# Kernel optimization log

Hardware: AMD Instinct MI355X
Metric: run time of the kernel (lower is better)

## Reference

```python
import jax, jax.numpy as jnp
from jax import lax
import numpy as np

B, L, D = 32, 128, 6          # programs, statements per program, tree depth
T = 2 ** D - 1                # nodes per statement tree (complete binary tree)
V, E, C, H = 50000, 128, 128, 256  # vocab, embed dim, encode dim, gru hidden


def setup_inputs():
    key = jax.random.key(0)
    ks = jax.random.split(key, 12)
    s = 0.05
    return {
        "tokens": jax.random.randint(ks[0], (B, L, T), 0, V),
        "emb": jax.random.normal(ks[1], (V, E), jnp.float32) * s,
        "Wc": jax.random.normal(ks[2], (C, E), jnp.float32) * s,
        "bc": jax.random.normal(ks[3], (C,), jnp.float32) * s,
        "Wih_f": jax.random.normal(ks[4], (3 * H, C), jnp.float32) * s,
        "Whh_f": jax.random.normal(ks[5], (3 * H, H), jnp.float32) * s,
        "bih_f": jax.random.normal(ks[6], (3 * H,), jnp.float32) * s,
        "bhh_f": jax.random.normal(ks[7], (3 * H,), jnp.float32) * s,
        "Wih_b": jax.random.normal(ks[8], (3 * H, C), jnp.float32) * s,
        "Whh_b": jax.random.normal(ks[9], (3 * H, H), jnp.float32) * s,
        "bih_b": jax.random.normal(ks[10], (3 * H,), jnp.float32) * s,
        "bhh_b": jax.random.normal(ks[11], (3 * H,), jnp.float32) * s,
    }


def _tree_encode(tokens, emb, Wc, bc):
    # h(node) = W_c(embed(tok)) + sum of children subtree encodings (W_l/W_r unused in source)
    h = jnp.einsum("blte,ce->bltc", emb[tokens], Wc) + bc  # [B,L,T,C]
    for d in range(D - 1, 0, -1):  # deepest level first
        start, n = 2 ** d - 1, 2 ** d
        ch = h[:, :, start:start + n, :]
        ch = ch.reshape(ch.shape[0], ch.shape[1], n // 2, 2, ch.shape[-1]).sum(3)
        p0 = 2 ** (d - 1) - 1
        h = h.at[:, :, p0:p0 + n // 2, :].add(ch)
    # max over all subtree encodings, with zeros included (batch_node starts at 0)
    return jnp.maximum(h.max(axis=2), 0.0)  # [B,L,C]


def _gru_dir(x, Wih, Whh, bih, bhh, reverse):
    # torch GRU gate order: r, z, n
    def step(hp, xt):
        gi = xt @ Wih.T + bih
        gh = hp @ Whh.T + bhh
        ir, iz, inn = jnp.split(gi, 3, -1)
        hr, hz, hn = jnp.split(gh, 3, -1)
        r = jax.nn.sigmoid(ir + hr)
        z = jax.nn.sigmoid(iz + hz)
        nn_ = jnp.tanh(inn + r * hn)
        hnew = (1.0 - z) * nn_ + z * hp
        return hnew, hnew
    xs = jnp.swapaxes(x, 0, 1)  # [L,B,C]
    h0 = jnp.zeros((x.shape[0], Whh.shape[1]), x.dtype)
    _, ys = lax.scan(step, h0, xs, reverse=reverse)
    return jnp.swapaxes(ys, 0, 1)  # [B,L,H]


def reference(tokens, emb, Wc, bc, Wih_f, Whh_f, bih_f, bhh_f, Wih_b, Whh_b, bih_b, bhh_b):
    enc = _tree_encode(tokens, emb, Wc, bc)                       # [B,L,C]
    fwd = _gru_dir(enc, Wih_f, Whh_f, bih_f, bhh_f, reverse=False)
    bwd = _gru_dir(enc, Wih_b, Whh_b, bih_b, bhh_b, reverse=True)
    gru_out = jnp.concatenate([fwd, bwd], axis=-1)                # [B,L,2H]
    return gru_out.max(axis=1)                                    # max-pool over time -> [B,2H]
```

## Files before the change

kernel.cpp:

```cpp
#include <hip/hip_runtime.h>
#include <hip/hip_bf16.h>
#include <hip/hip_fp16.h>
#include <math.h>

#define NV 50000
#define NE 128
#define NC 128
#define NH 256
#define NB 32
#define NL 128
#define NT 63
#define G3 768

typedef _Float16 half2_t __attribute__((ext_vector_type(2)));

__device__ __forceinline__ float sigmoidf_(float x) { return 1.0f / (1.0f + expf(-x)); }

__device__ __forceinline__ float fdot2_(unsigned int a, unsigned int b, float c) {
#if __has_builtin(__builtin_amdgcn_fdot2)
  return __builtin_amdgcn_fdot2(__builtin_bit_cast(half2_t, a),
                                __builtin_bit_cast(half2_t, b), c, false);
#else
  half2_t ah = __builtin_bit_cast(half2_t, a);
  half2_t bh = __builtin_bit_cast(half2_t, b);
  return fmaf((float)ah[0], (float)bh[0], fmaf((float)ah[1], (float)bh[1], c));
#endif
}

__global__ __launch_bounds__(256) void gemm_bt_k128(
    const float* __restrict__ A, const float* __restrict__ Bm,
    const float* __restrict__ bias, float* __restrict__ Cm,
    int M, int N) {
  __shared__ __align__(16) float As[64 * 129];
  __shared__ __align__(16) float BsT[128 * 132];
  const int m0 = blockIdx.x * 64;
  const int n0 = blockIdx.y * 128;
  const int tid = threadIdx.x;

#pragma unroll
  for (int i = 0; i < 32; ++i) {
    int e = tid + i * 256;
    int r = e >> 7, k = e & 127;
    int m = m0 + r;
    As[r * 129 + k] = (m < M) ? A[(size_t)m * 128 + k] : 0.0f;
  }
#pragma unroll
  for (int i = 0; i < 64; ++i) {
    int e = tid + i * 256;
    int n = e >> 7, k = e & 127;
    BsT[k * 132 + n] = Bm[(size_t)(n0 + n) * 128 + k];
  }
  __syncthreads();

  const int tn = tid & 15;
  const int tm = tid >> 4;
  const int ml = tm * 4, nl = tn * 8;

  float acc[4][8];
#pragma unroll
  for (int i = 0; i < 4; ++i)
#pragma unroll
    for (int j = 0; j < 8; ++j) acc[i][j] = 0.0f;

#pragma unroll 4
  for (int k = 0; k < 128; ++k) {
    float a0 = As[(ml + 0) * 129 + k];
    float a1 = As[(ml + 1) * 129 + k];
    float a2 = As[(ml + 2) * 129 + k];
    float a3 = As[(ml + 3) * 129 + k];
    float4 b0 = *(const float4*)&BsT[k * 132 + nl];
    float4 b1 = *(const float4*)&BsT[k * 132 + nl + 4];
    const float bv[8] = {b0.x, b0.y, b0.z, b0.w, b1.x, b1.y, b1.z, b1.w};
#pragma unroll
    for (int j = 0; j < 8; ++j) {
      acc[0][j] = fmaf(a0, bv[j], acc[0][j]);
      acc[1][j] = fmaf(a1, bv[j], acc[1][j]);
      acc[2][j] = fmaf(a2, bv[j], acc[2][j]);
      acc[3][j] = fmaf(a3, bv[j], acc[3][j]);
    }
  }

  float bv[8];
#pragma unroll
  for (int j = 0; j < 8; ++j) bv[j] = bias ? bias[n0 + nl + j] : 0.0f;

#pragma unroll
  for (int i = 0; i < 4; ++i) {
    int m = m0 + ml + i;
    if (m < M) {
      float* crow = &Cm[(size_t)m * N + n0 + nl];
#pragma unroll
      for (int j = 0; j < 8; ++j) crow[j] = acc[i][j] + bv[j];
    }
  }
}

__global__ __launch_bounds__(128) void tree_encode(
    const int* __restrict__ tokens, const float* __restrict__ P,
    const float* __restrict__ bc, float* __restrict__ enc) {
  __shared__ int toks[NT];
  const int blk = blockIdx.x;
  const int c = threadIdx.x;
  if (c < NT) toks[c] = tokens[(size_t)blk * NT + c];
  __syncthreads();

  float s[NT];
#pragma unroll
  for (int i = 0; i < NT; ++i) s[i] = P[(size_t)toks[i] * NC + c];
#pragma unroll
  for (int i = 30; i >= 0; --i) s[i] += s[2 * i + 1] + s[2 * i + 2];

  const float bcv = bc[c];
  float m = -1e30f;
#pragma unroll
  for (int i = 0; i < NT; ++i) {
    const float cnt = (i == 0) ? 63.0f
                    : (i < 3)  ? 31.0f
                    : (i < 7)  ? 15.0f
                    : (i < 15) ? 7.0f
                    : (i < 31) ? 3.0f
                               : 1.0f;
    m = fmaxf(m, s[i] + cnt * bcv);
  }
  enc[(size_t)blk * NC + c] = fmaxf(m, 0.0f);
}

__global__ __launch_bounds__(256) void conv_w_f16(
    const float* __restrict__ Wf, const float* __restrict__ Wb,
    unsigned int* __restrict__ out) {
  int i = blockIdx.x * 256 + threadIdx.x;
  if (i < G3 * (NH / 2)) {
    float2 a = ((const float2*)Wf)[i];
    __half2 ha = __floats2half2_rn(a.x, a.y);
    out[i] = *(unsigned int*)&ha;
    float2 b = ((const float2*)Wb)[i];
    __half2 hb = __floats2half2_rn(b.x, b.y);
    out[G3 * (NH / 2) + i] = *(unsigned int*)&hb;
  }
}

__global__ __launch_bounds__(768, 3) void gru_scan_reg(
    const unsigned int* __restrict__ Wh16, const float* __restrict__ GI,
    const float* __restrict__ bhh_f, const float* __restrict__ bhh_b,
    float* __restrict__ out) {
  const int dir = blockIdx.x >> 5;
  const int b = blockIdx.x & 31;
  const int tid = threadIdx.x;

  __shared__ __align__(16) unsigned int h16p[NH / 2];
  __shared__ float gh[G3];

  unsigned int w[128];
  {
    const uint4* wrow = (const uint4*)(Wh16 + ((size_t)dir * G3 + tid) * (NH / 2));
#pragma unroll
    for (int i = 0; i < 32; ++i) {
      uint4 v = wrow[i];
      w[4 * i + 0] = v.x; w[4 * i + 1] = v.y;
      w[4 * i + 2] = v.z; w[4 * i + 3] = v.w;
    }
  }

  const float* __restrict__ bhh = dir ? bhh_b : bhh_f;
  float br = 0.f, bz = 0.f, bn = 0.f, hreg = 0.f, hmax = -1e30f;
  if (tid < NH) {
    br = bhh[tid];
    bz = bhh[tid + NH];
    bn = bhh[tid + 2 * NH];
  }
  if (tid < NH / 2) h16p[tid] = 0u;
  const float* __restrict__ gi_base =
      GI + ((size_t)dir * NB * NL + (size_t)b * NL) * G3;
  __syncthreads();

  for (int st = 0; st < NL; ++st) {
    const int t = dir ? (NL - 1 - st) : st;
    float gir = 0.f, giz = 0.f, gin = 0.f;
    if (tid < NH) {
      const float* gi = gi_base + (size_t)t * G3;
      gir = gi[tid];
      giz = gi[tid + NH];
      gin = gi[tid + 2 * NH];
    }
    float acc = 0.0f;
    const uint4* h4 = (const uint4*)h16p;
#pragma unroll
    for (int k = 0; k < 32; ++k) {
      uint4 hv = h4[k];
      acc = fdot2_(w[4 * k + 0], hv.x, acc);
      acc = fdot2_(w[4 * k + 1], hv.y, acc);
      acc = fdot2_(w[4 * k + 2], hv.z, acc);
      acc = fdot2_(w[4 * k + 3], hv.w, acc);
    }
    gh[tid] = acc;
    __syncthreads();
    if (tid < NH) {
      float r = sigmoidf_(gir + gh[tid] + br);
      float z = sigmoidf_(giz + gh[tid + NH] + bz);
      float n = tanhf(gin + r * (gh[tid + 2 * NH] + bn));
      hreg = (1.0f - z) * n + z * hreg;
      hmax = fmaxf(hmax, hreg);
      ((unsigned short*)h16p)[tid] = __half_as_ushort(__float2half_rn(hreg));
    }
    __syncthreads();
  }
  if (tid < NH) out[(size_t)b * (2 * NH) + (size_t)dir * NH + tid] = hmax;
}

extern "C" void kernel_launch(void* const* d_in, const int* in_sizes, int n_in,
                              void* d_out, int out_size, void* d_ws, size_t ws_size,
                              hipStream_t stream) {
  const int*   tokens = (const int*)d_in[0];
  const float* emb    = (const float*)d_in[1];
  const float* Wc     = (const float*)d_in[2];
  const float* bc     = (const float*)d_in[3];
  const float* Wih_f  = (const float*)d_in[4];
  const float* Whh_f  = (const float*)d_in[5];
  const float* bih_f  = (const float*)d_in[6];
  const float* bhh_f  = (const float*)d_in[7];
  const float* Wih_b  = (const float*)d_in[8];
  const float* Whh_b  = (const float*)d_in[9];
  const float* bih_b  = (const float*)d_in[10];
  const float* bhh_b  = (const float*)d_in[11];
  float* out = (float*)d_out;

  float* P   = (float*)d_ws;
  float* enc = P + (size_t)NV * NC;
  float* GI  = enc + (size_t)NB * NL * NC;
  unsigned int* Wh16 = (unsigned int*)(GI + (size_t)2 * NB * NL * G3);

  conv_w_f16<<<dim3((G3 * (NH / 2) + 255) / 256), dim3(256), 0, stream>>>(
      Whh_f, Whh_b, Wh16);
  gemm_bt_k128<<<dim3((NV + 63) / 64, NC / 128), dim3(256), 0, stream>>>(
      emb, Wc, nullptr, P, NV, NC);
  tree_encode<<<dim3(NB * NL), dim3(128), 0, stream>>>(tokens, P, bc, enc);
  gemm_bt_k128<<<dim3(NB * NL / 64, G3 / 128), dim3(256), 0, stream>>>(
      enc, Wih_f, bih_f, GI, NB * NL, G3);
  gemm_bt_k128<<<dim3(NB * NL / 64, G3 / 128), dim3(256), 0, stream>>>(
      enc, Wih_b, bih_b, GI + (size_t)NB * NL * G3, NB * NL, G3);
  gru_scan_reg<<<dim3(64), dim3(768), 0, stream>>>(
      Wh16, GI, bhh_f, bhh_b, out);
}
```

Measured before the change: 355.3 us.

## Restructure GRU scan to fuse gate dot-products per unit with one barrier per step

The recurrent scan now uses 512 threads, with each pair of threads owning one hidden unit and splitting the K dimension in half. Each thread holds the r/z/n weight slices in registers, and the pair combines partial sums with a lane shuffle, so the gh shared-memory round trip and one of the two barriers per step go away. The hidden state is double-buffered in LDS, next-step GI values are prefetched, and the two input-projection GEMMs are merged into a single launch using the z grid dimension. This shortens the serial per-step critical path of the scan, at the cost of a new packed weight layout and 192 uint4 registers per thread.

```diff
diff --git a/kernel.cpp b/kernel.cpp
--- a/kernel.cpp
+++ b/kernel.cpp
@@ -4,7 +4,6 @@
 #include <math.h>
 
 #define NV 50000
-#define NE 128
 #define NC 128
 #define NH 256
 #define NB 32
@@ -95,6 +94,79 @@
   }
 }
 
+__global__ __launch_bounds__(256) void gemm_bt_k128_dual(
+    const float* __restrict__ A,
+    const float* __restrict__ B0, const float* __restrict__ B1,
+    const float* __restrict__ bias0, const float* __restrict__ bias1,
+    float* __restrict__ C0, float* __restrict__ C1, int M, int N) {
+  const float* __restrict__ Bm = blockIdx.z ? B1 : B0;
+  const float* __restrict__ bias = blockIdx.z ? bias1 : bias0;
+  float* __restrict__ Cm = blockIdx.z ? C1 : C0;
+
+  __shared__ __align__(16) float As[64 * 129];
+  __shared__ __align__(16) float BsT[128 * 132];
+  const int m0 = blockIdx.x * 64;
+  const int n0 = blockIdx.y * 128;
+  const int tid = threadIdx.x;
+
+#pragma unroll
+  for (int i = 0; i < 32; ++i) {
+    int e = tid + i * 256;
+    int r = e >> 7, k = e & 127;
+    int m = m0 + r;
+    As[r * 129 + k] = (m < M) ? A[(size_t)m * 128 + k] : 0.0f;
+  }
+#pragma unroll
+  for (int i = 0; i < 64; ++i) {
+    int e = tid + i * 256;
+    int n = e >> 7, k = e & 127;
+    BsT[k * 132 + n] = Bm[(size_t)(n0 + n) * 128 + k];
+  }
+  __syncthreads();
+
+  const int tn = tid & 15;
+  const int tm = tid >> 4;
+  const int ml = tm * 4, nl = tn * 8;
+
+  float acc[4][8];
+#pragma unroll
+  for (int i = 0; i < 4; ++i)
+#pragma unroll
+    for (int j = 0; j < 8; ++j) acc[i][j] = 0.0f;
+
+#pragma unroll 4
+  for (int k = 0; k < 128; ++k) {
+    float a0 = As[(ml + 0) * 129 + k];
+    float a1 = As[(ml + 1) * 129 + k];
+    float a2 = As[(ml + 2) * 129 + k];
+    float a3 = As[(ml + 3) * 129 + k];
+    float4 b0 = *(const float4*)&BsT[k * 132 + nl];
+    float4 b1 = *(const float4*)&BsT[k * 132 + nl + 4];
+    const float bv[8] = {b0.x, b0.y, b0.z, b0.w, b1.x, b1.y, b1.z, b1.w};
+#pragma unroll
+    for (int j = 0; j < 8; ++j) {
+      acc[0][j] = fmaf(a0, bv[j], acc[0][j]);
+      acc[1][j] = fmaf(a1, bv[j], acc[1][j]);
+      acc[2][j] = fmaf(a2, bv[j], acc[2][j]);
+      acc[3][j] = fmaf(a3, bv[j], acc[3][j]);
+    }
+  }
+
+  float bv[8];
+#pragma unroll
+  for (int j = 0; j < 8; ++j) bv[j] = bias[n0 + nl + j];
+
+#pragma unroll
+  for (int i = 0; i < 4; ++i) {
+    int m = m0 + ml + i;
+    if (m < M) {
+      float* crow = &Cm[(size_t)m * N + n0 + nl];
+#pragma unroll
+      for (int j = 0; j < 8; ++j) crow[j] = acc[i][j] + bv[j];
+    }
+  }
+}
+
 __global__ __launch_bounds__(128) void tree_encode(
     const int* __restrict__ tokens, const float* __restrict__ P,
     const float* __restrict__ bc, float* __restrict__ enc) {
@@ -125,86 +197,99 @@
   enc[(size_t)blk * NC + c] = fmaxf(m, 0.0f);
 }
 
-__global__ __launch_bounds__(256) void conv_w_f16(
+__global__ __launch_bounds__(256) void conv_w_pack(
     const float* __restrict__ Wf, const float* __restrict__ Wb,
-    unsigned int* __restrict__ out) {
+    uint4* __restrict__ out) {
   int i = blockIdx.x * 256 + threadIdx.x;
-  if (i < G3 * (NH / 2)) {
-    float2 a = ((const float2*)Wf)[i];
-    __half2 ha = __floats2half2_rn(a.x, a.y);
-    out[i] = *(unsigned int*)&ha;
-    float2 b = ((const float2*)Wb)[i];
-    __half2 hb = __floats2half2_rn(b.x, b.y);
-    out[G3 * (NH / 2) + i] = *(unsigned int*)&hb;
-  }
-}
-
-__global__ __launch_bounds__(768, 3) void gru_scan_reg(
-    const unsigned int* __restrict__ Wh16, const float* __restrict__ GI,
+  if (i >= 2 * 32 * G3) return;
+  int dir = i / (32 * G3);
+  int rem = i - dir * 32 * G3;
+  int kc = rem / G3;
+  int row = rem - kc * G3;
+  const float* __restrict__ W = dir ? Wb : Wf;
+  const float4 a = *(const float4*)&W[(size_t)row * NH + kc * 8];
+  const float4 b = *(const float4*)&W[(size_t)row * NH + kc * 8 + 4];
+  __half2 p0 = __floats2half2_rn(a.x, a.y);
+  __half2 p1 = __floats2half2_rn(a.z, a.w);
+  __half2 p2 = __floats2half2_rn(b.x, b.y);
+  __half2 p3 = __floats2half2_rn(b.z, b.w);
+  uint4 o;
+  o.x = *(unsigned int*)&p0; o.y = *(unsigned int*)&p1;
+  o.z = *(unsigned int*)&p2; o.w = *(unsigned int*)&p3;
+  out[i] = o;
+}
+
+__global__ __launch_bounds__(512, 2) void gru_scan_v4(
+    const uint4* __restrict__ Wpk, const float* __restrict__ GI,
     const float* __restrict__ bhh_f, const float* __restrict__ bhh_b,
     float* __restrict__ out) {
   const int dir = blockIdx.x >> 5;
   const int b = blockIdx.x & 31;
   const int tid = threadIdx.x;
-
-  __shared__ __align__(16) unsigned int h16p[NH / 2];
-  __shared__ float gh[G3];
-
-  unsigned int w[128];
-  {
-    const uint4* wrow = (const uint4*)(Wh16 + ((size_t)dir * G3 + tid) * (NH / 2));
-#pragma unroll
-    for (int i = 0; i < 32; ++i) {
-      uint4 v = wrow[i];
-      w[4 * i + 0] = v.x; w[4 * i + 1] = v.y;
-      w[4 * i + 2] = v.z; w[4 * i + 3] = v.w;
-    }
-  }
-
+  const int c = tid >> 1;
+  const int kh = tid & 1;
+
+  __shared__ __align__(16) uint4 hbuf[2][32];
+
+  const uint4* __restrict__ Wd = Wpk + (size_t)dir * 32 * G3;
+  uint4 wr[16], wz[16], wn[16];
+#pragma unroll
+  for (int j = 0; j < 16; ++j) {
+    const size_t base = (size_t)(kh * 16 + j) * G3 + c;
+    wr[j] = Wd[base];
+    wz[j] = Wd[base + NH];
+    wn[j] = Wd[base + 2 * NH];
+  }
   const float* __restrict__ bhh = dir ? bhh_b : bhh_f;
-  float br = 0.f, bz = 0.f, bn = 0.f, hreg = 0.f, hmax = -1e30f;
-  if (tid < NH) {
-    br = bhh[tid];
-    bz = bhh[tid + NH];
-    bn = bhh[tid + 2 * NH];
-  }
-  if (tid < NH / 2) h16p[tid] = 0u;
+  const float br = bhh[c], bz = bhh[c + NH], bn = bhh[c + 2 * NH];
+  if (tid < 32) ((uint4*)hbuf)[tid] = uint4{0u, 0u, 0u, 0u};
+
   const float* __restrict__ gi_base =
       GI + ((size_t)dir * NB * NL + (size_t)b * NL) * G3;
+  float gir, giz, gin;
+  {
+    const float* g = gi_base + (size_t)(dir ? NL - 1 : 0) * G3;
+    gir = g[c]; giz = g[c + NH]; gin = g[c + 2 * NH];
+  }
+  float hreg = 0.0f, hmax = -1e30f;
   __syncthreads();
 
   for (int st = 0; st < NL; ++st) {
-    const int t = dir ? (NL - 1 - st) : st;
-    float gir = 0.f, giz = 0.f, gin = 0.f;
-    if (tid < NH) {
-      const float* gi = gi_base + (size_t)t * G3;
-      gir = gi[tid];
-      giz = gi[tid + NH];
-      gin = gi[tid + 2 * NH];
-    }
-    float acc = 0.0f;
-    const uint4* h4 = (const uint4*)h16p;
-#pragma unroll
-    for (int k = 0; k < 32; ++k) {
-      uint4 hv = h4[k];
-      acc = fdot2_(w[4 * k + 0], hv.x, acc);
-      acc = fdot2_(w[4 * k + 1], hv.y, acc);
-      acc = fdot2_(w[4 * k + 2], hv.z, acc);
-      acc = fdot2_(w[4 * k + 3], hv.w, acc);
-    }
-    gh[tid] = acc;
+    float girN, gizN, ginN;
+    {
+      const int stn = (st + 1 < NL) ? st + 1 : st;
+      const int tn = dir ? (NL - 1 - stn) : stn;
+      const float* g = gi_base + (size_t)tn * G3;
+      girN = g[c]; gizN = g[c + NH]; ginN = g[c + 2 * NH];
+    }
+    const uint4* __restrict__ h4 = hbuf[st & 1] + kh * 16;
+    float ar = 0.f, az = 0.f, an = 0.f;
+#pragma unroll
+    for (int j = 0; j < 16; ++j) {
+      uint4 hv = h4[j];
+      ar = fdot2_(wr[j].x, hv.x, ar); ar = fdot2_(wr[j].y, hv.y, ar);
+      ar = fdot2_(wr[j].z, hv.z, ar); ar = fdot2_(wr[j].w, hv.w, ar);
+      az = fdot2_(wz[j].x, hv.x, az); az = fdot2_(wz[j].y, hv.y, az);
+      az = fdot2_(wz[j].z, hv.z, az); az = fdot2_(wz[j].w, hv.w, az);
+      an = fdot2_(wn[j].x, hv.x, an); an = fdot2_(wn[j].y, hv.y, an);
+      an = fdot2_(wn[j].z, hv.z, an); an = fdot2_(wn[j].w, hv.w, an);
+    }
+    ar += __shfl_xor(ar, 1);
+    az += __shfl_xor(az, 1);
+    an += __shfl_xor(an, 1);
+    float r = sigmoidf_(gir + ar + br);
+    float z = sigmoidf_(giz + az + bz);
+    float n = tanhf(gin + r * (an + bn));
+    hreg = (1.0f - z) * n + z * hreg;
+    hmax = fmaxf(hmax, hreg);
+    if (kh == 0) {
+      ((unsigned short*)hbuf[(st + 1) & 1])[c] =
+          __half_as_ushort(__float2half_rn(hreg));
+    }
     __syncthreads();
-    if (tid < NH) {
-      float r = sigmoidf_(gir + gh[tid] + br);
-      float z = sigmoidf_(giz + gh[tid + NH] + bz);
-      float n = tanhf(gin + r * (gh[tid + 2 * NH] + bn));
-      hreg = (1.0f - z) * n + z * hreg;
-      hmax = fmaxf(hmax, hreg);
-      ((unsigned short*)h16p)[tid] = __half_as_ushort(__float2half_rn(hreg));
-    }
-    __syncthreads();
-  }
-  if (tid < NH) out[(size_t)b * (2 * NH) + (size_t)dir * NH + tid] = hmax;
+    gir = girN; giz = gizN; gin = ginN;
+  }
+  if (kh == 0) out[(size_t)b * (2 * NH) + (size_t)dir * NH + c] = hmax;
 }
 
 extern "C" void kernel_launch(void* const* d_in, const int* in_sizes, int n_in,
@@ -227,17 +312,16 @@
   float* P   = (float*)d_ws;
   float* enc = P + (size_t)NV * NC;
   float* GI  = enc + (size_t)NB * NL * NC;
-  unsigned int* Wh16 = (unsigned int*)(GI + (size_t)2 * NB * NL * G3);
-
-  conv_w_f16<<<dim3((G3 * (NH / 2) + 255) / 256), dim3(256), 0, stream>>>(
-      Whh_f, Whh_b, Wh16);
+  uint4* Wpk = (uint4*)(GI + (size_t)2 * NB * NL * G3);
+
+  conv_w_pack<<<dim3((2 * 32 * G3 + 255) / 256), dim3(256), 0, stream>>>(
+      Whh_f, Whh_b, Wpk);
   gemm_bt_k128<<<dim3((NV + 63) / 64, NC / 128), dim3(256), 0, stream>>>(
       emb, Wc, nullptr, P, NV, NC);
   tree_encode<<<dim3(NB * NL), dim3(128), 0, stream>>>(tokens, P, bc, enc);
-  gemm_bt_k128<<<dim3(NB * NL / 64, G3 / 128), dim3(256), 0, stream>>>(
-      enc, Wih_f, bih_f, GI, NB * NL, G3);
-  gemm_bt_k128<<<dim3(NB * NL / 64, G3 / 128), dim3(256), 0, stream>>>(
-      enc, Wih_b, bih_b, GI + (size_t)NB * NL * G3, NB * NL, G3);
-  gru_scan_reg<<<dim3(64), dim3(768), 0, stream>>>(
-      Wh16, GI, bhh_f, bhh_b, out);
-}
+  gemm_bt_k128_dual<<<dim3(NB * NL / 64, G3 / 128, 2), dim3(256), 0, stream>>>(
+      enc, Wih_f, Wih_b, bih_f, bih_b,
+      GI, GI + (size_t)NB * NL * G3, NB * NL, G3);
+  gru_scan_v4<<<dim3(64), dim3(512), 0, stream>>>(
+      Wpk, GI, bhh_f, bhh_b, out);
+}
```

After: 324.3 us. -8.7%, faster.
